# Performance work log

Measured on AMD Instinct MI355X. Metric: run time of the kernel, lower is better.

Reference implementation:

```python
import jax, jax.numpy as jnp
from jax import lax
import numpy as np

B, T, H, P = 256, 2048, 256, 24

def setup_inputs() -> dict:
    key = jax.random.key(0)
    ks = jax.random.split(key, 7)
    s_ih = 1.0 / np.sqrt(H)
    return {
        "x": jax.random.normal(ks[0], (B, T, 1), dtype=jnp.float32),
        "W_ih": jax.random.normal(ks[1], (H, 1), dtype=jnp.float32) * s_ih,
        "W_hh": jax.random.normal(ks[2], (H, H), dtype=jnp.float32) * s_ih,
        "b_ih": jax.random.normal(ks[3], (H,), dtype=jnp.float32) * s_ih,
        "b_hh": jax.random.normal(ks[4], (H,), dtype=jnp.float32) * s_ih,
        "W_out": jax.random.normal(ks[5], (P, H), dtype=jnp.float32) * s_ih,
        "b_out": jax.random.normal(ks[6], (P,), dtype=jnp.float32) * s_ih,
    }

def reference(x, W_ih, W_hh, b_ih, b_hh, W_out, b_out):
    # Precompute input projection for all timesteps: [B,T,H]
    xp = jnp.einsum('bti,hi->bth', x, W_ih) + b_ih + b_hh
    h0 = jnp.zeros((x.shape[0], W_hh.shape[0]), dtype=x.dtype)

    def step(h, xt):  # xt: [B,H]
        h_new = jnp.tanh(xt + h @ W_hh.T)
        return h_new, None

    hT, _ = lax.scan(step, h0, xp.transpose(1, 0, 2))  # scan over T
    # Linear head on last hidden state: [B,P]
    return hT @ W_out.T + b_out
```

## Files before the change

kernel.cpp:

```cpp
#include <hip/hip_runtime.h>


#define BB 256
#define TT 2048
#define HH 256
#define PP 24
#define HSTR 20

typedef float v2f __attribute__((ext_vector_type(2)));

struct alignas(16) hquad { v2f lo, hi; };

__device__ __forceinline__ int hidx(int k) { return (k >> 4) * HSTR + (k & 15); }

template<int CTRL>
__device__ __forceinline__ float dppadd(float dst, float src) {
    return dst + __int_as_float(__builtin_amdgcn_update_dpp(
        0, __float_as_int(src), CTRL, 0xf, 0xf, true));
}

#define PKMUL(a, w, q) asm("v_pk_mul_f32 %0, %1, %2" : "=v"(a) : "v"(w), "v"(q))
#define PKFMA(a, w, q) asm("v_pk_fma_f32 %0, %1, %2, %0" : "+v"(a) : "v"(w), "v"(q))

__global__ __launch_bounds__(512, 2) __attribute__((amdgpu_waves_per_eu(2, 2)))
void rnn_persist(const float* __restrict__ x,
                 const float* __restrict__ W_ih,
                 const float* __restrict__ W_hh,
                 const float* __restrict__ b_ih,
                 const float* __restrict__ b_hh,
                 const float* __restrict__ W_out,
                 const float* __restrict__ b_out,
                 float* __restrict__ out)
{
    __shared__ __align__(16) float hbuf[2][16 * HSTR];

    const int tid = threadIdx.x;
    const int b   = blockIdx.x;
    const int c   = tid & 15;
    const int g   = tid >> 4;

    hbuf[0][hidx(tid & 255)] = 0.0f;

    const int m[8] = {0, 2, 7, 5, 8, 10, 15, 13};

    v2f w2[8][8];
    #pragma unroll
    for (int s = 0; s < 8; ++s) {
        const int row_idx = 8 * g + ((c ^ m[s]) >> 1);
        const float* row = W_hh + row_idx * HH + 16 * c;
        #pragma unroll
        for (int j = 0; j < 4; ++j) {
            const float4 q = *(const float4*)(row + 4 * j);
            w2[s][2 * j + 0] = (v2f){q.x, q.y};
            w2[s][2 * j + 1] = (v2f){q.z, q.w};
        }
    }

    const int   o_fin = 8 * g + (c >> 1);
    const float wih   = W_ih[o_fin];
    const float cb    = b_ih[o_fin] + b_hh[o_fin];
    const int   widx  = hidx(o_fin);

    __syncthreads();

    const float* hc0 = hbuf[0] + c * HSTR;
    const float* hc1 = hbuf[1] + c * HSTR;
    const float* xb  = x + b * TT;

    auto step = [&](const float* __restrict__ cur, float* __restrict__ nxt,
                    float xt) __attribute__((always_inline)) {
        const hquad* hq = (const hquad*)cur;
        const hquad q0 = hq[0], q1 = hq[1], q2 = hq[2], q3 = hq[3];

        v2f acc[8];
        #pragma unroll
        for (int s = 0; s < 8; ++s) PKMUL(acc[s], w2[s][0], q0.lo);
        #pragma unroll
        for (int s = 0; s < 8; ++s) PKFMA(acc[s], w2[s][1], q0.hi);
        #pragma unroll
        for (int s = 0; s < 8; ++s) PKFMA(acc[s], w2[s][2], q1.lo);
        #pragma unroll
        for (int s = 0; s < 8; ++s) PKFMA(acc[s], w2[s][3], q1.hi);
        #pragma unroll
        for (int s = 0; s < 8; ++s) PKFMA(acc[s], w2[s][4], q2.lo);
        #pragma unroll
        for (int s = 0; s < 8; ++s) PKFMA(acc[s], w2[s][5], q2.hi);
        #pragma unroll
        for (int s = 0; s < 8; ++s) PKFMA(acc[s], w2[s][6], q3.lo);
        #pragma unroll
        for (int s = 0; s < 8; ++s) PKFMA(acc[s], w2[s][7], q3.hi);

        float aa[8];
        #pragma unroll
        for (int s = 0; s < 8; ++s) aa[s] = acc[s].x + acc[s].y;

        float b0 = dppadd<0x128>(aa[0], aa[4]);
        float b1 = dppadd<0x128>(aa[1], aa[5]);
        float b2 = dppadd<0x128>(aa[2], aa[6]);
        float b3 = dppadd<0x128>(aa[3], aa[7]);
        float c0 = dppadd<0x141>(b0, b2);
        float c1 = dppadd<0x141>(b1, b3);
        float d  = dppadd<0x4E>(c0, c1);
        float e  = dppadd<0xB1>(d, d);

        const float u  = fmaf(xt, wih, cb) + e;
        const float p  = __builtin_amdgcn_exp2f(u * 2.8853900817779268f);
        const float th = fmaf(-2.f, __builtin_amdgcn_rcpf(p + 1.f), 1.f);
        nxt[widx] = th;
        __syncthreads();
    };

    float4 xa = *(const float4*)(xb + 0);
    float4 xc = *(const float4*)(xb + 4);
    for (int t = 0; t < TT; t += 8) {
        const int tn = (t + 8 < TT) ? (t + 8) : t;
        const float4 xa_n = *(const float4*)(xb + tn);
        const float4 xc_n = *(const float4*)(xb + tn + 4);
        step(hc0, hbuf[1], xa.x);
        step(hc1, hbuf[0], xa.y);
        step(hc0, hbuf[1], xa.z);
        step(hc1, hbuf[0], xa.w);
        step(hc0, hbuf[1], xc.x);
        step(hc1, hbuf[0], xc.y);
        step(hc0, hbuf[1], xc.z);
        step(hc1, hbuf[0], xc.w);
        xa = xa_n;
        xc = xc_n;
    }

    if (tid < PP) {
        const float* wo = W_out + tid * HH;
        float s0 = 0.f, s1 = 0.f, s2 = 0.f, s3 = 0.f;
        #pragma unroll
        for (int h = 0; h < HH; h += 4) {
            s0 = fmaf(wo[h + 0], hbuf[0][hidx(h + 0)], s0);
            s1 = fmaf(wo[h + 1], hbuf[0][hidx(h + 1)], s1);
            s2 = fmaf(wo[h + 2], hbuf[0][hidx(h + 2)], s2);
            s3 = fmaf(wo[h + 3], hbuf[0][hidx(h + 3)], s3);
        }
        out[b * PP + tid] = b_out[tid] + (s0 + s1) + (s2 + s3);
    }
}

extern "C" void kernel_launch(void* const* d_in, const int* in_sizes, int n_in,
                              void* d_out, int out_size, void* d_ws, size_t ws_size,
                              hipStream_t stream) {
    const float* x     = (const float*)d_in[0];
    const float* W_ih  = (const float*)d_in[1];
    const float* W_hh  = (const float*)d_in[2];
    const float* b_ih  = (const float*)d_in[3];
    const float* b_hh  = (const float*)d_in[4];
    const float* W_out = (const float*)d_in[5];
    const float* b_out = (const float*)d_in[6];
    float* out = (float*)d_out;

    rnn_persist<<<BB, 512, 0, stream>>>(x, W_ih, W_hh, b_ih, b_hh, W_out, b_out, out);
}
```

Before: 1.014 ms.

## Rewrite recurrent loop as hand-scheduled inline assembly with scalar x loads

Replaces the compiler-generated timestep loop with one large inline-asm block. It uses scalar FMAs instead of packed ones, ds_swizzle instead of DPP for the cross-lane reduction, scalar s_load of x in batches of 16, and explicit waitcnt/barrier placement. The goal is to remove compiler scheduling overhead and shorten the per-step latency chain. The cost is far more VALU instructions and LDS-latency swizzles in place of DPP adds, and launch bounds drop to one block per CU. Hardcoded registers and hazard nops also raise correctness risk.

```diff
diff --git a/kernel.cpp b/kernel.cpp
--- a/kernel.cpp
+++ b/kernel.cpp
@@ -7,22 +7,119 @@
 #define PP 24
 #define HSTR 20
 
-typedef float v2f __attribute__((ext_vector_type(2)));
-
-struct alignas(16) hquad { v2f lo, hi; };
-
 __device__ __forceinline__ int hidx(int k) { return (k >> 4) * HSTR + (k & 15); }
 
-template<int CTRL>
-__device__ __forceinline__ float dppadd(float dst, float src) {
-    return dst + __int_as_float(__builtin_amdgcn_update_dpp(
-        0, __float_as_int(src), CTRL, 0xf, 0xf, true));
-}
-
-#define PKMUL(a, w, q) asm("v_pk_mul_f32 %0, %1, %2" : "=v"(a) : "v"(w), "v"(q))
-#define PKFMA(a, w, q) asm("v_pk_fma_f32 %0, %1, %2, %0" : "+v"(a) : "v"(w), "v"(q))
-
-__global__ __launch_bounds__(512, 2) __attribute__((amdgpu_waves_per_eu(2, 2)))
+#define STEP(RD, WR, XS) \
+  "ds_read_b128 v[48:51], " RD "\n" \
+  "ds_read_b128 v[52:55], " RD " offset:16\n" \
+  "ds_read_b128 v[56:59], " RD " offset:32\n" \
+  "ds_read_b128 v[60:63], " RD " offset:48\n" \
+  "s_waitcnt lgkmcnt(3)\n" \
+  "v_mul_f32 v32, v64, v48\n"  "v_mul_f32 v40, v65, v49\n" \
+  "v_mul_f32 v33, v80, v48\n"  "v_mul_f32 v41, v81, v49\n" \
+  "v_mul_f32 v34, v96, v48\n"  "v_mul_f32 v42, v97, v49\n" \
+  "v_mul_f32 v35, v112, v48\n" "v_mul_f32 v43, v113, v49\n" \
+  "v_mul_f32 v36, v128, v48\n" "v_mul_f32 v44, v129, v49\n" \
+  "v_mul_f32 v37, v144, v48\n" "v_mul_f32 v45, v145, v49\n" \
+  "v_mul_f32 v38, v160, v48\n" "v_mul_f32 v46, v161, v49\n" \
+  "v_mul_f32 v39, v176, v48\n" "v_mul_f32 v47, v177, v49\n" \
+  "v_fma_f32 v32, v66, v50, v32\n"  "v_fma_f32 v40, v67, v51, v40\n" \
+  "v_fma_f32 v33, v82, v50, v33\n"  "v_fma_f32 v41, v83, v51, v41\n" \
+  "v_fma_f32 v34, v98, v50, v34\n"  "v_fma_f32 v42, v99, v51, v42\n" \
+  "v_fma_f32 v35, v114, v50, v35\n" "v_fma_f32 v43, v115, v51, v43\n" \
+  "v_fma_f32 v36, v130, v50, v36\n" "v_fma_f32 v44, v131, v51, v44\n" \
+  "v_fma_f32 v37, v146, v50, v37\n" "v_fma_f32 v45, v147, v51, v45\n" \
+  "v_fma_f32 v38, v162, v50, v38\n" "v_fma_f32 v46, v163, v51, v46\n" \
+  "v_fma_f32 v39, v178, v50, v39\n" "v_fma_f32 v47, v179, v51, v47\n" \
+  "s_waitcnt lgkmcnt(2)\n" \
+  "v_fma_f32 v32, v68, v52, v32\n"  "v_fma_f32 v40, v69, v53, v40\n" \
+  "v_fma_f32 v33, v84, v52, v33\n"  "v_fma_f32 v41, v85, v53, v41\n" \
+  "v_fma_f32 v34, v100, v52, v34\n" "v_fma_f32 v42, v101, v53, v42\n" \
+  "v_fma_f32 v35, v116, v52, v35\n" "v_fma_f32 v43, v117, v53, v43\n" \
+  "v_fma_f32 v36, v132, v52, v36\n" "v_fma_f32 v44, v133, v53, v44\n" \
+  "v_fma_f32 v37, v148, v52, v37\n" "v_fma_f32 v45, v149, v53, v45\n" \
+  "v_fma_f32 v38, v164, v52, v38\n" "v_fma_f32 v46, v165, v53, v46\n" \
+  "v_fma_f32 v39, v180, v52, v39\n" "v_fma_f32 v47, v181, v53, v47\n" \
+  "v_fma_f32 v32, v70, v54, v32\n"  "v_fma_f32 v40, v71, v55, v40\n" \
+  "v_fma_f32 v33, v86, v54, v33\n"  "v_fma_f32 v41, v87, v55, v41\n" \
+  "v_fma_f32 v34, v102, v54, v34\n" "v_fma_f32 v42, v103, v55, v42\n" \
+  "v_fma_f32 v35, v118, v54, v35\n" "v_fma_f32 v43, v119, v55, v43\n" \
+  "v_fma_f32 v36, v134, v54, v36\n" "v_fma_f32 v44, v135, v55, v44\n" \
+  "v_fma_f32 v37, v150, v54, v37\n" "v_fma_f32 v45, v151, v55, v45\n" \
+  "v_fma_f32 v38, v166, v54, v38\n" "v_fma_f32 v46, v167, v55, v46\n" \
+  "v_fma_f32 v39, v182, v54, v39\n" "v_fma_f32 v47, v183, v55, v47\n" \
+  "s_waitcnt lgkmcnt(1)\n" \
+  "v_fma_f32 v32, v72, v56, v32\n"  "v_fma_f32 v40, v73, v57, v40\n" \
+  "v_fma_f32 v33, v88, v56, v33\n"  "v_fma_f32 v41, v89, v57, v41\n" \
+  "v_fma_f32 v34, v104, v56, v34\n" "v_fma_f32 v42, v105, v57, v42\n" \
+  "v_fma_f32 v35, v120, v56, v35\n" "v_fma_f32 v43, v121, v57, v43\n" \
+  "v_fma_f32 v36, v136, v56, v36\n" "v_fma_f32 v44, v137, v57, v44\n" \
+  "v_fma_f32 v37, v152, v56, v37\n" "v_fma_f32 v45, v153, v57, v45\n" \
+  "v_fma_f32 v38, v168, v56, v38\n" "v_fma_f32 v46, v169, v57, v46\n" \
+  "v_fma_f32 v39, v184, v56, v39\n" "v_fma_f32 v47, v185, v57, v47\n" \
+  "v_fma_f32 v32, v74, v58, v32\n"  "v_fma_f32 v40, v75, v59, v40\n" \
+  "v_fma_f32 v33, v90, v58, v33\n"  "v_fma_f32 v41, v91, v59, v41\n" \
+  "v_fma_f32 v34, v106, v58, v34\n" "v_fma_f32 v42, v107, v59, v42\n" \
+  "v_fma_f32 v35, v122, v58, v35\n" "v_fma_f32 v43, v123, v59, v43\n" \
+  "v_fma_f32 v36, v138, v58, v36\n" "v_fma_f32 v44, v139, v59, v44\n" \
+  "v_fma_f32 v37, v154, v58, v37\n" "v_fma_f32 v45, v155, v59, v45\n" \
+  "v_fma_f32 v38, v170, v58, v38\n" "v_fma_f32 v46, v171, v59, v46\n" \
+  "v_fma_f32 v39, v186, v58, v39\n" "v_fma_f32 v47, v187, v59, v47\n" \
+  "s_waitcnt lgkmcnt(0)\n" \
+  "v_fma_f32 v32, v76, v60, v32\n"  "v_fma_f32 v40, v77, v61, v40\n" \
+  "v_fma_f32 v33, v92, v60, v33\n"  "v_fma_f32 v41, v93, v61, v41\n" \
+  "v_fma_f32 v34, v108, v60, v34\n" "v_fma_f32 v42, v109, v61, v42\n" \
+  "v_fma_f32 v35, v124, v60, v35\n" "v_fma_f32 v43, v125, v61, v43\n" \
+  "v_fma_f32 v36, v140, v60, v36\n" "v_fma_f32 v44, v141, v61, v44\n" \
+  "v_fma_f32 v37, v156, v60, v37\n" "v_fma_f32 v45, v157, v61, v45\n" \
+  "v_fma_f32 v38, v172, v60, v38\n" "v_fma_f32 v46, v173, v61, v46\n" \
+  "v_fma_f32 v39, v188, v60, v39\n" "v_fma_f32 v47, v189, v61, v47\n" \
+  "v_fma_f32 v32, v78, v62, v32\n"  "v_fma_f32 v40, v79, v63, v40\n" \
+  "v_fma_f32 v33, v94, v62, v33\n"  "v_fma_f32 v41, v95, v63, v41\n" \
+  "v_fma_f32 v34, v110, v62, v34\n" "v_fma_f32 v42, v111, v63, v42\n" \
+  "v_fma_f32 v35, v126, v62, v35\n" "v_fma_f32 v43, v127, v63, v43\n" \
+  "v_fma_f32 v36, v142, v62, v36\n" "v_fma_f32 v44, v143, v63, v44\n" \
+  "v_fma_f32 v37, v158, v62, v37\n" "v_fma_f32 v45, v159, v63, v45\n" \
+  "v_fma_f32 v38, v174, v62, v38\n" "v_fma_f32 v46, v175, v63, v46\n" \
+  "v_fma_f32 v39, v190, v62, v39\n" "v_fma_f32 v47, v191, v63, v47\n" \
+   \
+  "v_add_f32 v24, v32, v40\n" "v_add_f32 v25, v33, v41\n" \
+  "v_add_f32 v26, v34, v42\n" "v_add_f32 v27, v35, v43\n" \
+  "v_add_f32 v28, v36, v44\n" "v_add_f32 v29, v37, v45\n" \
+  "v_add_f32 v30, v38, v46\n" "v_add_f32 v31, v39, v47\n" \
+   \
+  "ds_swizzle_b32 v33, v28 offset:0x201F\n" \
+  "ds_swizzle_b32 v34, v29 offset:0x201F\n" \
+  "ds_swizzle_b32 v35, v30 offset:0x201F\n" \
+  "ds_swizzle_b32 v36, v31 offset:0x201F\n" \
+  "s_waitcnt lgkmcnt(0)\n" \
+  "v_add_f32 v24, v24, v33\n" "v_add_f32 v25, v25, v34\n" \
+  "v_add_f32 v26, v26, v35\n" "v_add_f32 v27, v27, v36\n" \
+  "ds_swizzle_b32 v33, v26 offset:0x1C1F\n" \
+  "ds_swizzle_b32 v34, v27 offset:0x1C1F\n" \
+  "s_waitcnt lgkmcnt(0)\n" \
+  "v_add_f32 v24, v24, v33\n" "v_add_f32 v25, v25, v34\n" \
+  "ds_swizzle_b32 v33, v25 offset:0x081F\n" \
+  "s_waitcnt lgkmcnt(0)\n" \
+  "v_add_f32 v24, v24, v33\n" \
+  "ds_swizzle_b32 v33, v24 offset:0x041F\n" \
+  "s_waitcnt lgkmcnt(0)\n" \
+  "v_fma_f32 v25, " XS ", %[wih], %[cb]\n" \
+  "v_add_f32 v24, v24, v33\n" \
+   \
+  "v_add_f32 v24, v25, v24\n" \
+  "v_mul_f32 v24, 0x4038aa3b, v24\n" \
+  "v_exp_f32 v24, v24\n" \
+  "s_nop 3\n" \
+  "v_add_f32 v24, 1.0, v24\n" \
+  "v_rcp_f32 v24, v24\n" \
+  "s_nop 3\n" \
+  "v_fma_f32 v24, -2.0, v24, 1.0\n" \
+  "ds_write_b32 " WR ", v24\n" \
+  "s_waitcnt lgkmcnt(0)\n" \
+  "s_barrier\n"
+
+__global__ __launch_bounds__(512, 1)
 void rnn_persist(const float* __restrict__ x,
                  const float* __restrict__ W_ih,
                  const float* __restrict__ W_hh,
@@ -43,90 +140,119 @@
 
     const int m[8] = {0, 2, 7, 5, 8, 10, 15, 13};
 
-    v2f w2[8][8];
+    unsigned woff[8];
     #pragma unroll
     for (int s = 0; s < 8; ++s) {
         const int row_idx = 8 * g + ((c ^ m[s]) >> 1);
-        const float* row = W_hh + row_idx * HH + 16 * c;
-        #pragma unroll
-        for (int j = 0; j < 4; ++j) {
-            const float4 q = *(const float4*)(row + 4 * j);
-            w2[s][2 * j + 0] = (v2f){q.x, q.y};
-            w2[s][2 * j + 1] = (v2f){q.z, q.w};
-        }
+        woff[s] = (unsigned)((row_idx * HH + 16 * c) * 4);
     }
 
     const int   o_fin = 8 * g + (c >> 1);
     const float wih   = W_ih[o_fin];
     const float cb    = b_ih[o_fin] + b_hh[o_fin];
-    const int   widx  = hidx(o_fin);
+
+    const unsigned rd0 = (unsigned)(uintptr_t)(&hbuf[0][c * HSTR]);
+    const unsigned rd1 = (unsigned)(uintptr_t)(&hbuf[1][c * HSTR]);
+    const unsigned wr0 = (unsigned)(uintptr_t)(&hbuf[0][hidx(o_fin)]);
+    const unsigned wr1 = (unsigned)(uintptr_t)(&hbuf[1][hidx(o_fin)]);
+
+    const float* xb = x + b * TT;
 
     __syncthreads();
 
-    const float* hc0 = hbuf[0] + c * HSTR;
-    const float* hc1 = hbuf[1] + c * HSTR;
-    const float* xb  = x + b * TT;
-
-    auto step = [&](const float* __restrict__ cur, float* __restrict__ nxt,
-                    float xt) __attribute__((always_inline)) {
-        const hquad* hq = (const hquad*)cur;
-        const hquad q0 = hq[0], q1 = hq[1], q2 = hq[2], q3 = hq[3];
-
-        v2f acc[8];
-        #pragma unroll
-        for (int s = 0; s < 8; ++s) PKMUL(acc[s], w2[s][0], q0.lo);
-        #pragma unroll
-        for (int s = 0; s < 8; ++s) PKFMA(acc[s], w2[s][1], q0.hi);
-        #pragma unroll
-        for (int s = 0; s < 8; ++s) PKFMA(acc[s], w2[s][2], q1.lo);
-        #pragma unroll
-        for (int s = 0; s < 8; ++s) PKFMA(acc[s], w2[s][3], q1.hi);
-        #pragma unroll
-        for (int s = 0; s < 8; ++s) PKFMA(acc[s], w2[s][4], q2.lo);
-        #pragma unroll
-        for (int s = 0; s < 8; ++s) PKFMA(acc[s], w2[s][5], q2.hi);
-        #pragma unroll
-        for (int s = 0; s < 8; ++s) PKFMA(acc[s], w2[s][6], q3.lo);
-        #pragma unroll
-        for (int s = 0; s < 8; ++s) PKFMA(acc[s], w2[s][7], q3.hi);
-
-        float aa[8];
-        #pragma unroll
-        for (int s = 0; s < 8; ++s) aa[s] = acc[s].x + acc[s].y;
-
-        float b0 = dppadd<0x128>(aa[0], aa[4]);
-        float b1 = dppadd<0x128>(aa[1], aa[5]);
-        float b2 = dppadd<0x128>(aa[2], aa[6]);
-        float b3 = dppadd<0x128>(aa[3], aa[7]);
-        float c0 = dppadd<0x141>(b0, b2);
-        float c1 = dppadd<0x141>(b1, b3);
-        float d  = dppadd<0x4E>(c0, c1);
-        float e  = dppadd<0xB1>(d, d);
-
-        const float u  = fmaf(xt, wih, cb) + e;
-        const float p  = __builtin_amdgcn_exp2f(u * 2.8853900817779268f);
-        const float th = fmaf(-2.f, __builtin_amdgcn_rcpf(p + 1.f), 1.f);
-        nxt[widx] = th;
-        __syncthreads();
-    };
-
-    float4 xa = *(const float4*)(xb + 0);
-    float4 xc = *(const float4*)(xb + 4);
-    for (int t = 0; t < TT; t += 8) {
-        const int tn = (t + 8 < TT) ? (t + 8) : t;
-        const float4 xa_n = *(const float4*)(xb + tn);
-        const float4 xc_n = *(const float4*)(xb + tn + 4);
-        step(hc0, hbuf[1], xa.x);
-        step(hc1, hbuf[0], xa.y);
-        step(hc0, hbuf[1], xa.z);
-        step(hc1, hbuf[0], xa.w);
-        step(hc0, hbuf[1], xc.x);
-        step(hc1, hbuf[0], xc.y);
-        step(hc0, hbuf[1], xc.z);
-        step(hc1, hbuf[0], xc.w);
-        xa = xa_n;
-        xc = xc_n;
-    }
+    asm volatile(
+        "global_load_dwordx4 v[64:67],   %[o0], %[wb]\n"
+        "global_load_dwordx4 v[68:71],   %[o0], %[wb] offset:16\n"
+        "global_load_dwordx4 v[72:75],   %[o0], %[wb] offset:32\n"
+        "global_load_dwordx4 v[76:79],   %[o0], %[wb] offset:48\n"
+        "global_load_dwordx4 v[80:83],   %[o1], %[wb]\n"
+        "global_load_dwordx4 v[84:87],   %[o1], %[wb] offset:16\n"
+        "global_load_dwordx4 v[88:91],   %[o1], %[wb] offset:32\n"
+        "global_load_dwordx4 v[92:95],   %[o1], %[wb] offset:48\n"
+        "global_load_dwordx4 v[96:99],   %[o2], %[wb]\n"
+        "global_load_dwordx4 v[100:103], %[o2], %[wb] offset:16\n"
+        "global_load_dwordx4 v[104:107], %[o2], %[wb] offset:32\n"
+        "global_load_dwordx4 v[108:111], %[o2], %[wb] offset:48\n"
+        "global_load_dwordx4 v[112:115], %[o3], %[wb]\n"
+        "global_load_dwordx4 v[116:119], %[o3], %[wb] offset:16\n"
+        "global_load_dwordx4 v[120:123], %[o3], %[wb] offset:32\n"
+        "global_load_dwordx4 v[124:127], %[o3], %[wb] offset:48\n"
+        "global_load_dwordx4 v[128:131], %[o4], %[wb]\n"
+        "global_load_dwordx4 v[132:135], %[o4], %[wb] offset:16\n"
+        "global_load_dwordx4 v[136:139], %[o4], %[wb] offset:32\n"
+        "global_load_dwordx4 v[140:143], %[o4], %[wb] offset:48\n"
+        "global_load_dwordx4 v[144:147], %[o5], %[wb]\n"
+        "global_load_dwordx4 v[148:151], %[o5], %[wb] offset:16\n"
+        "global_load_dwordx4 v[152:155], %[o5], %[wb] offset:32\n"
+        "global_load_dwordx4 v[156:159], %[o5], %[wb] offset:48\n"
+        "global_load_dwordx4 v[160:163], %[o6], %[wb]\n"
+        "global_load_dwordx4 v[164:167], %[o6], %[wb] offset:16\n"
+        "global_load_dwordx4 v[168:171], %[o6], %[wb] offset:32\n"
+        "global_load_dwordx4 v[172:175], %[o6], %[wb] offset:48\n"
+        "global_load_dwordx4 v[176:179], %[o7], %[wb]\n"
+        "global_load_dwordx4 v[180:183], %[o7], %[wb] offset:16\n"
+        "global_load_dwordx4 v[184:187], %[o7], %[wb] offset:32\n"
+        "global_load_dwordx4 v[188:191], %[o7], %[wb] offset:48\n"
+        "s_mov_b64 s[16:17], %[xp]\n"
+        "s_movk_i32 s20, 0x80\n"
+        "s_waitcnt vmcnt(0)\n"
+        "L_outer_%=:\n"
+        "s_load_dwordx16 s[24:39], s[16:17], 0x0\n"
+        "s_add_u32 s16, s16, 64\n"
+        "s_addc_u32 s17, s17, 0\n"
+        "s_waitcnt lgkmcnt(0)\n"
+        "s_movk_i32 s22, 4\n"
+        "L_inner_%=:\n"
+        STEP("%[r0]", "%[w1]", "s24")
+        STEP("%[r1]", "%[w0]", "s25")
+        STEP("%[r0]", "%[w1]", "s26")
+        STEP("%[r1]", "%[w0]", "s27")
+        "s_mov_b64 s[24:25], s[28:29]\n"
+        "s_mov_b64 s[26:27], s[30:31]\n"
+        "s_mov_b64 s[28:29], s[32:33]\n"
+        "s_mov_b64 s[30:31], s[34:35]\n"
+        "s_mov_b64 s[32:33], s[36:37]\n"
+        "s_mov_b64 s[34:35], s[38:39]\n"
+        "s_sub_u32 s22, s22, 1\n"
+        "s_cmp_lg_u32 s22, 0\n"
+        "s_cbranch_scc1 L_inner_%=\n"
+        "s_sub_u32 s20, s20, 1\n"
+        "s_cmp_lg_u32 s20, 0\n"
+        "s_cbranch_scc1 L_outer_%=\n"
+        :
+        : [o0]"v"(woff[0]), [o1]"v"(woff[1]), [o2]"v"(woff[2]), [o3]"v"(woff[3]),
+          [o4]"v"(woff[4]), [o5]"v"(woff[5]), [o6]"v"(woff[6]), [o7]"v"(woff[7]),
+          [r0]"v"(rd0), [r1]"v"(rd1), [w0]"v"(wr0), [w1]"v"(wr1),
+          [wih]"v"(wih), [cb]"v"(cb),
+          [wb]"s"(W_hh), [xp]"s"(xb)
+        : "memory", "scc",
+          "s16","s17","s20","s22",
+          "s24","s25","s26","s27","s28","s29","s30","s31",
+          "s32","s33","s34","s35","s36","s37","s38","s39",
+          "v24","v25","v26","v27","v28","v29","v30","v31",
+          "v32","v33","v34","v35","v36","v37","v38","v39",
+          "v40","v41","v42","v43","v44","v45","v46","v47",
+          "v48","v49","v50","v51","v52","v53","v54","v55",
+          "v56","v57","v58","v59","v60","v61","v62","v63",
+          "v64","v65","v66","v67","v68","v69","v70","v71",
+          "v72","v73","v74","v75","v76","v77","v78","v79",
+          "v80","v81","v82","v83","v84","v85","v86","v87",
+          "v88","v89","v90","v91","v92","v93","v94","v95",
+          "v96","v97","v98","v99","v100","v101","v102","v103",
+          "v104","v105","v106","v107","v108","v109","v110","v111",
+          "v112","v113","v114","v115","v116","v117","v118","v119",
+          "v120","v121","v122","v123","v124","v125","v126","v127",
+          "v128","v129","v130","v131","v132","v133","v134","v135",
+          "v136","v137","v138","v139","v140","v141","v142","v143",
+          "v144","v145","v146","v147","v148","v149","v150","v151",
+          "v152","v153","v154","v155","v156","v157","v158","v159",
+          "v160","v161","v162","v163","v164","v165","v166","v167",
+          "v168","v169","v170","v171","v172","v173","v174","v175",
+          "v176","v177","v178","v179","v180","v181","v182","v183",
+          "v184","v185","v186","v187","v188","v189","v190","v191"
+    );
+
+    __syncthreads();
 
     if (tid < PP) {
         const float* wo = W_out + tid * HH;
```

Result: slower. 1.231 ms (+21.4%).
